# Optimization experiments

Measured on AMD Instinct MI355X. Metric: run time of the kernel, lower is better.

The kernel has to match this reference:

```python
import jax, jax.numpy as jnp
import numpy as np

B, T, E = 4, 1024, 1024
H, MULT = 16, 2
HD = E // H
SCALE = HD ** -0.5


def setup_inputs() -> dict:
    key = jax.random.key(0)
    ks = jax.random.split(key, 9)
    s = 0.02
    return {
        "hidden_states": jax.random.normal(ks[0], (B, T, E), jnp.float32),
        "attention_mask": jnp.zeros((B, 1, T, T), jnp.float32),
        "Wq": jax.random.normal(ks[1], (E, E), jnp.float32) * s,
        "bq": jnp.zeros((E,), jnp.float32),
        "Wk": jax.random.normal(ks[2], (MULT * E, E), jnp.float32) * s,
        "bk": jnp.zeros((MULT * E,), jnp.float32),
        "Wv": jax.random.normal(ks[3], (MULT * E, E), jnp.float32) * s,
        "bv": jnp.zeros((MULT * E,), jnp.float32),
        "Wo": jax.random.normal(ks[4], (E, E), jnp.float32) * s,
        "bo": jnp.zeros((E,), jnp.float32),
    }


def reference(hidden_states, attention_mask, Wq, bq, Wk, bk, Wv, bv, Wo, bo):
    x = hidden_states  # [B, T, E]
    # q projection, scaled
    q = (jnp.einsum("bte,fe->btf", x, Wq) + bq) * SCALE  # [B,T,E]
    q = q.reshape(B, T, H, HD).transpose(0, 2, 1, 3)      # [B,H,T,HD]
    # k/v project to multiplier-expanded dim, then _shape with seq_len=-1:
    # [B,T,MULT*E] -> view(B, T*MULT, H, HD) (torch view semantics) -> [B,H,T*MULT,HD]
    k = jnp.einsum("bte,fe->btf", x, Wk) + bk             # [B,T,MULT*E]
    k = k.reshape(B, T * MULT, H, HD).transpose(0, 2, 1, 3)
    v = jnp.einsum("bte,fe->btf", x, Wv) + bv
    v = v.reshape(B, T * MULT, H, HD).transpose(0, 2, 1, 3)

    S = T * MULT  # src_len; src_len0 = T
    attn = jnp.einsum("bhtd,bhsd->bhts", q, k)            # [B,H,T,S]
    # custom mask broadcast: view src as [MULT, src_len0] and add mask[:, :, :, None, :]
    attn = attn.reshape(B, H, T, MULT, T) + attention_mask[:, :, :, None, :]
    attn = attn.reshape(B, H, T, S)
    attn = jax.nn.softmax(attn, axis=-1)
    out = jnp.einsum("bhts,bhsd->bhtd", attn, v)          # [B,H,T,HD]
    out = out.transpose(0, 2, 1, 3).reshape(B, T, E)
    out = jnp.einsum("bte,fe->btf", out, Wo) + bo
    return out
```

## Files before the change

kernel.cpp:

```cpp
#include <hip/hip_runtime.h>
#include <math.h>

#define BB    4
#define TT    1024
#define EE    1024
#define HH    16
#define HDIM  64
#define SS    2048
#define MROWS 4096
#define QSCALE 0.18033688011112f
#define LOG2E  1.4426950408889634f

typedef short  s8v  __attribute__((ext_vector_type(8)));
typedef float  f4v  __attribute__((ext_vector_type(4)));

__device__ __forceinline__ unsigned short f2bf(float f) {
    union { float f; unsigned u; } c; c.f = f;
    unsigned u = c.u + 0x7FFFu + ((c.u >> 16) & 1u);
    return (unsigned short)(u >> 16);
}
__device__ __forceinline__ float bflo(unsigned u) {
    union { unsigned u; float f; } c; c.u = u << 16; return c.f;
}
__device__ __forceinline__ float bfhi(unsigned u) {
    union { unsigned u; float f; } c; c.u = u & 0xffff0000u; return c.f;
}

__device__ __forceinline__ void async16(const void* g, void* l) {
    __builtin_amdgcn_global_load_lds(
        (const __attribute__((address_space(1))) unsigned int*)g,
        (__attribute__((address_space(3))) unsigned int*)l,
        16, 0, 0);
}

__global__ __launch_bounds__(256) void cvt6_kernel(
    const float* __restrict__ x,  const float* __restrict__ wq,
    const float* __restrict__ wk, const float* __restrict__ wv,
    const float* __restrict__ wo, const float* __restrict__ mk,
    unsigned short* __restrict__ xb,  unsigned short* __restrict__ wqb,
    unsigned short* __restrict__ wkb, unsigned short* __restrict__ wvb,
    unsigned short* __restrict__ wob, unsigned short* __restrict__ mbb)
{
    const int total = 3670016;
    int i = blockIdx.x * 256 + threadIdx.x;
    const int stride = gridDim.x * 256;
    for (; i < total; i += stride) {
        const float* s; unsigned short* d; int off; float sc = 1.0f;
        if (i < 1048576)      { s = x;  d = xb;  off = i; }
        else if (i < 1310720) { s = wq; d = wqb; off = i - 1048576; }
        else if (i < 1835008) { s = wk; d = wkb; off = i - 1310720; }
        else if (i < 2359296) { s = wv; d = wvb; off = i - 1835008; }
        else if (i < 2621440) { s = wo; d = wob; off = i - 2359296; }
        else                  { s = mk; d = mbb; off = i - 2621440; sc = LOG2E; }
        float4 v = ((const float4*)s)[off];
        ushort4 o;
        o.x = f2bf(v.x * sc); o.y = f2bf(v.y * sc);
        o.z = f2bf(v.z * sc); o.w = f2bf(v.w * sc);
        ((ushort4*)d)[off] = o;
    }
}

__global__ __launch_bounds__(256, 3) void gemm_qkv_kernel(
    const unsigned short* __restrict__ X,  const unsigned short* __restrict__ Wq,
    const unsigned short* __restrict__ Wk, const unsigned short* __restrict__ Wv,
    const float* __restrict__ bq, const float* __restrict__ bk,
    const float* __restrict__ bv, unsigned short* __restrict__ qp,
    unsigned short* __restrict__ kp, unsigned short* __restrict__ vt)
{
    __shared__ __align__(16) unsigned short As[128 * 32];
    __shared__ __align__(16) unsigned short Bs[128 * 32];

    const int tid = threadIdx.x;
    const int lane = tid & 63, w = tid >> 6;
    const int wm = (w & 1) * 64, wn = (w >> 1) * 64;
    const int col16 = lane & 15, quad = lane >> 4;
    const int y = blockIdx.y;
    const int part = (y < 8) ? 0 : (y < 24) ? 1 : 2;

    int am0, wn0;
    const unsigned short *Apan, *Wpan;
    if (part == 0) {
        am0 = blockIdx.x * 128; wn0 = y * 128;
        Apan = X + (size_t)am0 * EE;  Wpan = Wq + (size_t)wn0 * EE;
    } else if (part == 1) {
        am0 = blockIdx.x * 128; wn0 = (y - 8) * 128;
        Apan = X + (size_t)am0 * EE;  Wpan = Wk + (size_t)wn0 * EE;
    } else {
        am0 = (y - 24) * 128; wn0 = blockIdx.x * 128;
        Apan = Wv + (size_t)am0 * EE; Wpan = X + (size_t)wn0 * EE;
    }

    f4v acc[4][4];
#pragma unroll
    for (int i = 0; i < 4; ++i)
#pragma unroll
        for (int j = 0; j < 4; ++j) acc[i][j] = (f4v)0.0f;

    for (int k0 = 0; k0 < EE; k0 += 32) {
#pragma unroll
        for (int it = 0; it < 2; ++it) {
            int f = (it * 4 + w) * 64 + lane;
            int r = f >> 2, g = (f & 3) * 8;
            async16(Apan + (size_t)r * EE + k0 + g, As + (it * 4 + w) * 512);
            async16(Wpan + (size_t)r * EE + k0 + g, Bs + (it * 4 + w) * 512);
        }
        __syncthreads();
        s8v af[4], bf[4];
#pragma unroll
        for (int i = 0; i < 4; ++i)
            af[i] = *(const s8v*)(As + (wm + i * 16 + col16) * 32 + quad * 8);
#pragma unroll
        for (int j = 0; j < 4; ++j)
            bf[j] = *(const s8v*)(Bs + (wn + j * 16 + col16) * 32 + quad * 8);
#pragma unroll
        for (int i = 0; i < 4; ++i)
#pragma unroll
            for (int j = 0; j < 4; ++j)
                acc[i][j] = __builtin_amdgcn_mfma_f32_16x16x32_bf16(
                    af[i], bf[j], acc[i][j], 0, 0, 0);
        __syncthreads();
    }

#pragma unroll
    for (int j = 0; j < 4; ++j) {
        const int n = wn0 + wn + j * 16 + col16;
        const float bn = (part == 0) ? bq[n] : (part == 1) ? bk[n] : 0.0f;
#pragma unroll
        for (int i = 0; i < 4; ++i) {
            const int mb = am0 + wm + i * 16 + quad * 4;
#pragma unroll
            for (int r = 0; r < 4; ++r) {
                const int m = mb + r;
                if (part == 0) {
                    float c = acc[i][j][r] + bn;
                    qp[(size_t)m * EE + n] = f2bf(c * QSCALE);
                } else if (part == 1) {
                    float c = acc[i][j][r] + bn;
                    const int mm = n >> 10, h = (n >> 6) & 15, d = n & 63;
                    const int b_ = m >> 10, t = m & 1023;
                    const int s = 2 * t + mm;
                    kp[((size_t)(b_ * HH + h) * SS + s) * HDIM + d] = f2bf(c);
                } else {
                    float c = acc[i][j][r] + bv[m];
                    const int mm = m >> 10, h = (m >> 6) & 15, d = m & 63;
                    const int b_ = n >> 10, t = n & 1023;
                    const int s = 2 * t + mm;
                    vt[((size_t)(b_ * HH + h) * HDIM + d) * SS + s] = f2bf(c);
                }
            }
        }
    }
}

template <int Ksz, int Nsz, int BM, int BN>
__global__ __launch_bounds__(256, 4) void gemm_out_kernel(
    const unsigned short* __restrict__ A, const unsigned short* __restrict__ W,
    const float* __restrict__ bias, float* __restrict__ Cout)
{
    constexpr int WM = BM / 2, WN = BN / 2;
    constexpr int MI = WM / 16, NJ = WN / 16;
    __shared__ __align__(16) unsigned short As[BM * 32];
    __shared__ __align__(16) unsigned short Bs[BN * 32];

    const int tid = threadIdx.x;
    const int lane = tid & 63, w = tid >> 6;
    const int wm = (w & 1) * WM, wn = (w >> 1) * WN;
    const int col16 = lane & 15, quad = lane >> 4;
    const int m0 = blockIdx.x * BM;
    const int n0 = blockIdx.y * BN;

    f4v acc[MI][NJ];
#pragma unroll
    for (int i = 0; i < MI; ++i)
#pragma unroll
        for (int j = 0; j < NJ; ++j) acc[i][j] = (f4v)0.0f;

    for (int k0 = 0; k0 < Ksz; k0 += 32) {
#pragma unroll
        for (int it = 0; it < BM / 64; ++it) {
            int f = (it * 4 + w) * 64 + lane;
            int r = f >> 2, g = (f & 3) * 8;
            async16(A + (size_t)(m0 + r) * Ksz + k0 + g, As + (it * 4 + w) * 512);
        }
#pragma unroll
        for (int it = 0; it < BN / 64; ++it) {
            int f = (it * 4 + w) * 64 + lane;
            int r = f >> 2, g = (f & 3) * 8;
            async16(W + (size_t)(n0 + r) * Ksz + k0 + g, Bs + (it * 4 + w) * 512);
        }
        __syncthreads();
        s8v af[MI], bf[NJ];
#pragma unroll
        for (int i = 0; i < MI; ++i)
            af[i] = *(const s8v*)(As + (wm + i * 16 + col16) * 32 + quad * 8);
#pragma unroll
        for (int j = 0; j < NJ; ++j)
            bf[j] = *(const s8v*)(Bs + (wn + j * 16 + col16) * 32 + quad * 8);
#pragma unroll
        for (int i = 0; i < MI; ++i)
#pragma unroll
            for (int j = 0; j < NJ; ++j)
                acc[i][j] = __builtin_amdgcn_mfma_f32_16x16x32_bf16(
                    af[i], bf[j], acc[i][j], 0, 0, 0);
        __syncthreads();
    }

#pragma unroll
    for (int j = 0; j < NJ; ++j) {
        const int n = n0 + wn + j * 16 + col16;
        const float bn = bias[n];
#pragma unroll
        for (int i = 0; i < MI; ++i) {
            const int mb = m0 + wm + i * 16 + quad * 4;
#pragma unroll
            for (int r = 0; r < 4; ++r) {
                const int m = mb + r;
                Cout[(size_t)m * Nsz + n] = acc[i][j][r] + bn;
            }
        }
    }
}

__global__ __launch_bounds__(256, 4) void attn_mfma5_kernel(
    const unsigned short* __restrict__ Q, const unsigned short* __restrict__ Kh,
    const unsigned short* __restrict__ Vt, const unsigned short* __restrict__ Mb,
    unsigned short* __restrict__ O)
{
    constexpr int PT = 68;
    __shared__ __align__(16) unsigned short K0[64 * PT];
    __shared__ __align__(16) unsigned short K1[64 * PT];
    __shared__ __align__(16) unsigned short V0[64 * PT];
    __shared__ __align__(16) unsigned short V1[64 * PT];

    const int tid = threadIdx.x;
    const int lane = tid & 63, w = tid >> 6;
    const int col16 = lane & 15, quad = lane >> 4;

    const int gid = blockIdx.x;
    const int v = gid & 7, j = gid >> 3;
    const int bh = v * 8 + (j >> 4);
    const int t0 = (j & 15) * 64;
    const int b_ = bh >> 4, h = bh & 15;

    const unsigned short* Qrow =
        Q + (size_t)(b_ * TT + t0 + w * 16 + col16) * EE + h * HDIM;
    const s8v qf0 = *(const s8v*)(Qrow + quad * 8);
    const s8v qf1 = *(const s8v*)(Qrow + 32 + quad * 8);

    f4v oacc[4];
#pragma unroll
    for (int jd = 0; jd < 4; ++jd) oacc[jd] = (f4v)0.0f;
    float mrun = -INFINITY;
    f4v l4 = (f4v)0.0f;

    const unsigned short* Kb   = Kh + (size_t)bh * SS * HDIM;
    const unsigned short* Vb   = Vt + (size_t)bh * HDIM * SS;
    const unsigned short* Mrow = Mb + (size_t)b_ * TT * TT
                               + (size_t)(t0 + w * 16 + col16) * TT;
    const int myrow = (w * 16 + col16) * PT;
    const int r0 = tid >> 3, c0 = (tid & 7) * 8;

    uint4 kA0, kA1, kB0, kB1;
    uint4 vA0, vA1, vB0, vB1;
    uint2 mA0, mA1, mA2, mA3;

#define PREF_K(T2B)                                                            \
    kA0 = *(const uint4*)(Kb + (size_t)((T2B) + r0) * HDIM + c0);              \
    kA1 = *(const uint4*)(Kb + (size_t)((T2B) + r0 + 32) * HDIM + c0);         \
    kB0 = *(const uint4*)(Kb + (size_t)(1024 + (T2B) + r0) * HDIM + c0);       \
    kB1 = *(const uint4*)(Kb + (size_t)(1024 + (T2B) + r0 + 32) * HDIM + c0);
#define PREF_V(T2B)                                                            \
    vA0 = *(const uint4*)(Vb + (size_t)r0 * SS + (T2B) + c0);                  \
    vA1 = *(const uint4*)(Vb + (size_t)(r0 + 32) * SS + (T2B) + c0);           \
    vB0 = *(const uint4*)(Vb + (size_t)r0 * SS + 1024 + (T2B) + c0);           \
    vB1 = *(const uint4*)(Vb + (size_t)(r0 + 32) * SS + 1024 + (T2B) + c0);
#define PREF_M(T2B)                                                            \
    mA0 = *(const uint2*)(Mrow + (T2B) + 0 * 16 + quad * 4);                   \
    mA1 = *(const uint2*)(Mrow + (T2B) + 1 * 16 + quad * 4);                   \
    mA2 = *(const uint2*)(Mrow + (T2B) + 2 * 16 + quad * 4);                   \
    mA3 = *(const uint2*)(Mrow + (T2B) + 3 * 16 + quad * 4);

    PREF_K(0)
    PREF_V(0)
    PREF_M(0)

    for (int it16 = 0; it16 < 16; ++it16) {
        __syncthreads();

        *(uint4*)(K0 + r0 * PT + c0)        = kA0;
        *(uint4*)(K0 + (r0 + 32) * PT + c0) = kA1;
        *(uint4*)(K1 + r0 * PT + c0)        = kB0;
        *(uint4*)(K1 + (r0 + 32) * PT + c0) = kB1;
        *(uint4*)(V0 + r0 * PT + c0)        = vA0;
        *(uint4*)(V0 + (r0 + 32) * PT + c0) = vA1;
        *(uint4*)(V1 + r0 * PT + c0)        = vB0;
        *(uint4*)(V1 + (r0 + 32) * PT + c0) = vB1;

        f4v s0acc[4], s1acc[4];
        {
            f4v mv;
            mv[0] = bflo(mA0.x); mv[1] = bfhi(mA0.x);
            mv[2] = bflo(mA0.y); mv[3] = bfhi(mA0.y);
            s0acc[0] = mv; s1acc[0] = mv;
            mv[0] = bflo(mA1.x); mv[1] = bfhi(mA1.x);
            mv[2] = bflo(mA1.y); mv[3] = bfhi(mA1.y);
            s0acc[1] = mv; s1acc[1] = mv;
            mv[0] = bflo(mA2.x); mv[1] = bfhi(mA2.x);
            mv[2] = bflo(mA2.y); mv[3] = bfhi(mA2.y);
            s0acc[2] = mv; s1acc[2] = mv;
            mv[0] = bflo(mA3.x); mv[1] = bfhi(mA3.x);
            mv[2] = bflo(mA3.y); mv[3] = bfhi(mA3.y);
            s0acc[3] = mv; s1acc[3] = mv;
        }

        const int t2n = ((it16 + 1) & 15) * 64;
        PREF_K(t2n)
        PREF_M(t2n)

        __syncthreads();

        __builtin_amdgcn_s_setprio(1);
#pragma unroll
        for (int ks = 0; ks < 2; ++ks) {
            const s8v bq_ = ks ? qf1 : qf0;
#pragma unroll
            for (int js = 0; js < 4; ++js) {
                s8v ak0 = *(const s8v*)(K0 + (js * 16 + col16) * PT + ks * 32 + quad * 8);
                s8v ak1 = *(const s8v*)(K1 + (js * 16 + col16) * PT + ks * 32 + quad * 8);
                s0acc[js] = __builtin_amdgcn_mfma_f32_16x16x32_bf16(ak0, bq_, s0acc[js], 0, 0, 0);
                s1acc[js] = __builtin_amdgcn_mfma_f32_16x16x32_bf16(ak1, bq_, s1acc[js], 0, 0, 0);
            }
        }
        __builtin_amdgcn_s_setprio(0);

        float tm0 = fmaxf(fmaxf(s0acc[0][0], s0acc[0][1]), fmaxf(s0acc[0][2], s0acc[0][3]));
        float tm1 = fmaxf(fmaxf(s0acc[1][0], s0acc[1][1]), fmaxf(s0acc[1][2], s0acc[1][3]));
        float tm2 = fmaxf(fmaxf(s0acc[2][0], s0acc[2][1]), fmaxf(s0acc[2][2], s0acc[2][3]));
        float tm3 = fmaxf(fmaxf(s0acc[3][0], s0acc[3][1]), fmaxf(s0acc[3][2], s0acc[3][3]));
        float tn0 = fmaxf(fmaxf(s1acc[0][0], s1acc[0][1]), fmaxf(s1acc[0][2], s1acc[0][3]));
        float tn1 = fmaxf(fmaxf(s1acc[1][0], s1acc[1][1]), fmaxf(s1acc[1][2], s1acc[1][3]));
        float tn2 = fmaxf(fmaxf(s1acc[2][0], s1acc[2][1]), fmaxf(s1acc[2][2], s1acc[2][3]));
        float tn3 = fmaxf(fmaxf(s1acc[3][0], s1acc[3][1]), fmaxf(s1acc[3][2], s1acc[3][3]));
        float tmax = fmaxf(fmaxf(fmaxf(tm0, tm1), fmaxf(tm2, tm3)),
                           fmaxf(fmaxf(tn0, tn1), fmaxf(tn2, tn3)));

        if (!__all(tmax - mrun <= 10.0f)) {
            float tfull = fmaxf(tmax, __shfl_xor(tmax, 16));
            tfull = fmaxf(tfull, __shfl_xor(tfull, 32));
            const float mnew = fmaxf(mrun, tfull);
            const float scl = __builtin_amdgcn_exp2f(mrun - mnew);
            l4 *= scl;
            float sclr[4];
#pragma unroll
            for (int r = 0; r < 4; ++r) sclr[r] = __shfl(scl, quad * 4 + r);
#pragma unroll
            for (int jd = 0; jd < 4; ++jd)
#pragma unroll
                for (int r = 0; r < 4; ++r) oacc[jd][r] *= sclr[r];
            mrun = mnew;
        }

        unsigned pk0[8], pk1[8];
#pragma unroll
        for (int js = 0; js < 4; ++js) {
            f4v p0 = s0acc[js] - mrun;
            f4v p1 = s1acc[js] - mrun;
#pragma unroll
            for (int r = 0; r < 4; ++r) {
                p0[r] = __builtin_amdgcn_exp2f(p0[r]);
                p1[r] = __builtin_amdgcn_exp2f(p1[r]);
            }
            l4 += p0 + p1;
            __asm__("v_cvt_pk_bf16_f32 %0, %1, %2" : "=v"(pk0[js*2])   : "v"(p0[0]), "v"(p0[1]));
            __asm__("v_cvt_pk_bf16_f32 %0, %1, %2" : "=v"(pk0[js*2+1]) : "v"(p0[2]), "v"(p0[3]));
            __asm__("v_cvt_pk_bf16_f32 %0, %1, %2" : "=v"(pk1[js*2])   : "v"(p1[0]), "v"(p1[1]));
            __asm__("v_cvt_pk_bf16_f32 %0, %1, %2" : "=v"(pk1[js*2+1]) : "v"(p1[2]), "v"(p1[3]));
        }

        PREF_V(t2n)

        __syncthreads();

#pragma unroll
        for (int js = 0; js < 4; ++js) {
            *(uint2*)(K0 + myrow + js * 16 + quad * 4) = make_uint2(pk0[js*2], pk0[js*2+1]);
            *(uint2*)(K1 + myrow + js * 16 + quad * 4) = make_uint2(pk1[js*2], pk1[js*2+1]);
        }

        __builtin_amdgcn_s_setprio(1);
#pragma unroll
        for (int ks = 0; ks < 2; ++ks) {
            s8v p0 = *(const s8v*)(K0 + myrow + ks * 32 + quad * 8);
            s8v p1 = *(const s8v*)(K1 + myrow + ks * 32 + quad * 8);
#pragma unroll
            for (int jd = 0; jd < 4; ++jd) {
                s8v v0_ = *(const s8v*)(V0 + (jd * 16 + col16) * PT + ks * 32 + quad * 8);
                s8v v1_ = *(const s8v*)(V1 + (jd * 16 + col16) * PT + ks * 32 + quad * 8);
                oacc[jd] = __builtin_amdgcn_mfma_f32_16x16x32_bf16(p0, v0_, oacc[jd], 0, 0, 0);
                oacc[jd] = __builtin_amdgcn_mfma_f32_16x16x32_bf16(p1, v1_, oacc[jd], 0, 0, 0);
            }
        }
        __builtin_amdgcn_s_setprio(0);
    }
#undef PREF_K
#undef PREF_V
#undef PREF_M

    float lr = l4[0] + l4[1] + l4[2] + l4[3];
    lr += __shfl_xor(lr, 16);
    lr += __shfl_xor(lr, 32);
    const float inv = 1.0f / lr;
    float invr[4];
#pragma unroll
    for (int r = 0; r < 4; ++r) invr[r] = __shfl(inv, quad * 4 + r);
#pragma unroll
    for (int r = 0; r < 4; ++r) {
        const int t = t0 + w * 16 + quad * 4 + r;
#pragma unroll
        for (int jd = 0; jd < 4; ++jd)
            O[(size_t)(b_ * TT + t) * EE + h * HDIM + jd * 16 + col16] =
                f2bf(oacc[jd][r] * invr[r]);
    }
}

extern "C" void kernel_launch(void* const* d_in, const int* in_sizes, int n_in,
                              void* d_out, int out_size, void* d_ws, size_t ws_size,
                              hipStream_t stream)
{
    (void)in_sizes; (void)n_in; (void)out_size; (void)ws_size;

    const float* x    = (const float*)d_in[0];
    const float* mask = (const float*)d_in[1];
    const float* Wq   = (const float*)d_in[2];
    const float* bq   = (const float*)d_in[3];
    const float* Wk   = (const float*)d_in[4];
    const float* bk   = (const float*)d_in[5];
    const float* Wv   = (const float*)d_in[6];
    const float* bv   = (const float*)d_in[7];
    const float* Wo   = (const float*)d_in[8];
    const float* bo   = (const float*)d_in[9];
    float* out = (float*)d_out;

    unsigned short* xb  = (unsigned short*)d_ws;
    unsigned short* wqb = xb  + (size_t)MROWS * EE;
    unsigned short* wkb = wqb + (size_t)EE * EE;
    unsigned short* wvb = wkb + (size_t)2 * EE * EE;
    unsigned short* wob = wvb + (size_t)2 * EE * EE;
    unsigned short* mb  = wob + (size_t)EE * EE;
    unsigned short* qp  = mb  + (size_t)BB * TT * TT;
    unsigned short* kp  = qp  + (size_t)MROWS * EE;
    unsigned short* vt  = kp  + (size_t)BB * HH * SS * HDIM;
    unsigned short* ao  = vt  + (size_t)BB * HH * SS * HDIM;

    dim3 blk(256);

    cvt6_kernel<<<4096, blk, 0, stream>>>(x, Wq, Wk, Wv, Wo, mask,
                                          xb, wqb, wkb, wvb, wob, mb);
    gemm_qkv_kernel<<<dim3(32, 40), blk, 0, stream>>>(
        xb, wqb, wkb, wvb, bq, bk, bv, qp, kp, vt);
    attn_mfma5_kernel<<<dim3(1024), blk, 0, stream>>>(qp, kp, vt, mb, ao);
    gemm_out_kernel<EE, EE, 128, 64><<<dim3(32, 16), blk, 0, stream>>>(
        ao, wob, bo, out);
}
```

Before: 267.4 us.

## Store K/V in natural GEMM layout and reindex attention loads and mask

```diff
diff --git a/kernel.cpp b/kernel.cpp
--- a/kernel.cpp
+++ b/kernel.cpp
@@ -60,7 +60,7 @@
     }
 }
 
-__global__ __launch_bounds__(256, 3) void gemm_qkv_kernel(
+__global__ __launch_bounds__(256, 4) void gemm_qkv_kernel(
     const unsigned short* __restrict__ X,  const unsigned short* __restrict__ Wq,
     const unsigned short* __restrict__ Wk, const unsigned short* __restrict__ Wv,
     const float* __restrict__ bq, const float* __restrict__ bk,
@@ -132,20 +132,11 @@
             for (int r = 0; r < 4; ++r) {
                 const int m = mb + r;
                 if (part == 0) {
-                    float c = acc[i][j][r] + bn;
-                    qp[(size_t)m * EE + n] = f2bf(c * QSCALE);
+                    qp[(size_t)m * EE + n] = f2bf((acc[i][j][r] + bn) * QSCALE);
                 } else if (part == 1) {
-                    float c = acc[i][j][r] + bn;
-                    const int mm = n >> 10, h = (n >> 6) & 15, d = n & 63;
-                    const int b_ = m >> 10, t = m & 1023;
-                    const int s = 2 * t + mm;
-                    kp[((size_t)(b_ * HH + h) * SS + s) * HDIM + d] = f2bf(c);
+                    kp[(size_t)m * 2048 + n] = f2bf(acc[i][j][r] + bn);
                 } else {
-                    float c = acc[i][j][r] + bv[m];
-                    const int mm = m >> 10, h = (m >> 6) & 15, d = m & 63;
-                    const int b_ = n >> 10, t = n & 1023;
-                    const int s = 2 * t + mm;
-                    vt[((size_t)(b_ * HH + h) * HDIM + d) * SS + s] = f2bf(c);
+                    vt[(size_t)m * 4096 + n] = f2bf(acc[i][j][r] + bv[m]);
                 }
             }
         }
@@ -221,8 +212,8 @@
     }
 }
 
-__global__ __launch_bounds__(256, 4) void attn_mfma5_kernel(
-    const unsigned short* __restrict__ Q, const unsigned short* __restrict__ Kh,
+__global__ __launch_bounds__(256, 4) void attn_mfma12_kernel(
+    const unsigned short* __restrict__ Q, const unsigned short* __restrict__ Kp,
     const unsigned short* __restrict__ Vt, const unsigned short* __restrict__ Mb,
     unsigned short* __restrict__ O)
 {
@@ -253,8 +244,10 @@
     float mrun = -INFINITY;
     f4v l4 = (f4v)0.0f;
 
-    const unsigned short* Kb   = Kh + (size_t)bh * SS * HDIM;
-    const unsigned short* Vb   = Vt + (size_t)bh * HDIM * SS;
+    const unsigned short* Kb0 = Kp + (size_t)(b_ * 1024) * 2048 + h * 64;
+    const unsigned short* Kb1 = Kb0 + 1024;
+    const unsigned short* Vb0 = Vt + (size_t)(h * 64) * 4096 + b_ * 1024;
+    const unsigned short* Vb1 = Vb0 + (size_t)1024 * 4096;
     const unsigned short* Mrow = Mb + (size_t)b_ * TT * TT
                                + (size_t)(t0 + w * 16 + col16) * TT;
     const int myrow = (w * 16 + col16) * PT;
@@ -262,23 +255,26 @@
 
     uint4 kA0, kA1, kB0, kB1;
     uint4 vA0, vA1, vB0, vB1;
-    uint2 mA0, mA1, mA2, mA3;
+    uint4 mA0, mA1, mA2, mA3;
 
 #define PREF_K(T2B)                                                            \
-    kA0 = *(const uint4*)(Kb + (size_t)((T2B) + r0) * HDIM + c0);              \
-    kA1 = *(const uint4*)(Kb + (size_t)((T2B) + r0 + 32) * HDIM + c0);         \
-    kB0 = *(const uint4*)(Kb + (size_t)(1024 + (T2B) + r0) * HDIM + c0);       \
-    kB1 = *(const uint4*)(Kb + (size_t)(1024 + (T2B) + r0 + 32) * HDIM + c0);
+    kA0 = *(const uint4*)(Kb0 + (size_t)((T2B) + r0) * 2048 + c0);             \
+    kA1 = *(const uint4*)(Kb0 + (size_t)((T2B) + r0 + 32) * 2048 + c0);        \
+    kB0 = *(const uint4*)(Kb1 + (size_t)((T2B) + r0) * 2048 + c0);             \
+    kB1 = *(const uint4*)(Kb1 + (size_t)((T2B) + r0 + 32) * 2048 + c0);
 #define PREF_V(T2B)                                                            \
-    vA0 = *(const uint4*)(Vb + (size_t)r0 * SS + (T2B) + c0);                  \
-    vA1 = *(const uint4*)(Vb + (size_t)(r0 + 32) * SS + (T2B) + c0);           \
-    vB0 = *(const uint4*)(Vb + (size_t)r0 * SS + 1024 + (T2B) + c0);           \
-    vB1 = *(const uint4*)(Vb + (size_t)(r0 + 32) * SS + 1024 + (T2B) + c0);
+    vA0 = *(const uint4*)(Vb0 + (size_t)r0 * 4096 + (T2B) + c0);               \
+    vA1 = *(const uint4*)(Vb0 + (size_t)(r0 + 32) * 4096 + (T2B) + c0);        \
+    vB0 = *(const uint4*)(Vb1 + (size_t)r0 * 4096 + (T2B) + c0);               \
+    vB1 = *(const uint4*)(Vb1 + (size_t)(r0 + 32) * 4096 + (T2B) + c0);
 #define PREF_M(T2B)                                                            \
-    mA0 = *(const uint2*)(Mrow + (T2B) + 0 * 16 + quad * 4);                   \
-    mA1 = *(const uint2*)(Mrow + (T2B) + 1 * 16 + quad * 4);                   \
-    mA2 = *(const uint2*)(Mrow + (T2B) + 2 * 16 + quad * 4);                   \
-    mA3 = *(const uint2*)(Mrow + (T2B) + 3 * 16 + quad * 4);
+    {                                                                          \
+        const unsigned short* Mx = Mrow + ((2 * (T2B)) & 1023);                \
+        mA0 = *(const uint4*)(Mx + 0 * 32 + quad * 8);                         \
+        mA1 = *(const uint4*)(Mx + 1 * 32 + quad * 8);                         \
+        mA2 = *(const uint4*)(Mx + 2 * 32 + quad * 8);                         \
+        mA3 = *(const uint4*)(Mx + 3 * 32 + quad * 8);                         \
+    }
 
     PREF_K(0)
     PREF_V(0)
@@ -299,18 +295,22 @@
         f4v s0acc[4], s1acc[4];
         {
             f4v mv;
-            mv[0] = bflo(mA0.x); mv[1] = bfhi(mA0.x);
-            mv[2] = bflo(mA0.y); mv[3] = bfhi(mA0.y);
-            s0acc[0] = mv; s1acc[0] = mv;
-            mv[0] = bflo(mA1.x); mv[1] = bfhi(mA1.x);
-            mv[2] = bflo(mA1.y); mv[3] = bfhi(mA1.y);
-            s0acc[1] = mv; s1acc[1] = mv;
-            mv[0] = bflo(mA2.x); mv[1] = bfhi(mA2.x);
-            mv[2] = bflo(mA2.y); mv[3] = bfhi(mA2.y);
-            s0acc[2] = mv; s1acc[2] = mv;
-            mv[0] = bflo(mA3.x); mv[1] = bfhi(mA3.x);
-            mv[2] = bflo(mA3.y); mv[3] = bfhi(mA3.y);
-            s0acc[3] = mv; s1acc[3] = mv;
+            mv[0] = bflo(mA0.x); mv[1] = bflo(mA0.y);
+            mv[2] = bflo(mA0.z); mv[3] = bflo(mA0.w); s0acc[0] = mv;
+            mv[0] = bfhi(mA0.x); mv[1] = bfhi(mA0.y);
+            mv[2] = bfhi(mA0.z); mv[3] = bfhi(mA0.w); s1acc[0] = mv;
+            mv[0] = bflo(mA1.x); mv[1] = bflo(mA1.y);
+            mv[2] = bflo(mA1.z); mv[3] = bflo(mA1.w); s0acc[1] = mv;
+            mv[0] = bfhi(mA1.x); mv[1] = bfhi(mA1.y);
+            mv[2] = bfhi(mA1.z); mv[3] = bfhi(mA1.w); s1acc[1] = mv;
+            mv[0] = bflo(mA2.x); mv[1] = bflo(mA2.y);
+            mv[2] = bflo(mA2.z); mv[3] = bflo(mA2.w); s0acc[2] = mv;
+            mv[0] = bfhi(mA2.x); mv[1] = bfhi(mA2.y);
+            mv[2] = bfhi(mA2.z); mv[3] = bfhi(mA2.w); s1acc[2] = mv;
+            mv[0] = bflo(mA3.x); mv[1] = bflo(mA3.y);
+            mv[2] = bflo(mA3.z); mv[3] = bflo(mA3.w); s0acc[3] = mv;
+            mv[0] = bfhi(mA3.x); mv[1] = bfhi(mA3.y);
+            mv[2] = bfhi(mA3.z); mv[3] = bfhi(mA3.w); s1acc[3] = mv;
         }
 
         const int t2n = ((it16 + 1) & 15) * 64;
@@ -458,7 +458,7 @@
                                           xb, wqb, wkb, wvb, wob, mb);
     gemm_qkv_kernel<<<dim3(32, 40), blk, 0, stream>>>(
         xb, wqb, wkb, wvb, bq, bk, bv, qp, kp, vt);
-    attn_mfma5_kernel<<<dim3(1024), blk, 0, stream>>>(qp, kp, vt, mb, ao);
+    attn_mfma12_kernel<<<dim3(1024), blk, 0, stream>>>(qp, kp, vt, mb, ao);
     gemm_out_kernel<EE, EE, 128, 64><<<dim3(32, 16), blk, 0, stream>>>(
         ao, wob, bo, out);
 }
```

After: 266.8 us. No clear change (-0.2%).
